# Kernel tuning notes

Measured on AMD Instinct MI355X. Metric: run time of the kernel, lower is better.

## Reference

```python
import jax, jax.numpy as jnp
import numpy as np

N = 2048        # tokens (batch*seq)
H = 4096        # hidden_size (LLaMA-7B)
I = 11008       # intermediate_size (LLaMA-7B)
QMAX = 127.0    # int8 symmetric quant range


def setup_inputs() -> dict:
    key = jax.random.key(0)
    ks = jax.random.split(key, 6)
    # pre-quantized int8 activations (stored as int32) + per-token dynamic scales
    x_q = jax.random.randint(ks[0], (N, H), -127, 128, dtype=jnp.int32)
    x_scale = jax.random.uniform(ks[1], (N,), dtype=jnp.float32) * 0.01 + 1e-4
    # fused [gate; up] int8 weight [2I, H] with per-output-channel scales
    w_gateup = jax.random.randint(ks[2], (2 * I, H), -127, 128, dtype=jnp.int32)
    w_gateup_scale = jax.random.uniform(ks[3], (2 * I,), dtype=jnp.float32) * 0.005 + 1e-4
    # down_proj int8 weight [H, I] with per-output-channel scales
    w_down = jax.random.randint(ks[4], (H, I), -127, 128, dtype=jnp.int32)
    w_down_scale = jax.random.uniform(ks[5], (H,), dtype=jnp.float32) * 0.005 + 1e-4
    return {"x_q": x_q, "x_scale": x_scale, "w_gateup": w_gateup,
            "w_gateup_scale": w_gateup_scale, "w_down": w_down,
            "w_down_scale": w_down_scale}


def reference(x_q, x_scale, w_gateup, w_gateup_scale, w_down, w_down_scale):
    acc = jnp.matmul(x_q, w_gateup.T)                      # [N, 2I] int32
    gateup = acc.astype(jnp.float32) * x_scale[:, None] * w_gateup_scale[None, :]
    # --- fused silu_and_mul + dynamic per-token requantization ---
    gate, up = jnp.split(gateup, 2, axis=-1)               # each [N, I]
    act = jax.nn.silu(gate) * up                           # [N, I]
    s2 = jnp.max(jnp.abs(act), axis=-1) / QMAX             # [N] dynamic scale
    q2 = jnp.clip(jnp.round(act / s2[:, None]), -QMAX, QMAX)  # requantized int8 (as f32)
    out = jnp.matmul(q2, w_down.T.astype(jnp.float32)) * s2[:, None] * w_down_scale[None, :]
    return out                                             # [N, H]
```

## Files before the change

### kernel.cpp

```cpp
#include <hip/hip_runtime.h>
#include <stdint.h>

typedef int i32x4 __attribute__((ext_vector_type(4)));
typedef unsigned short u16x8 __attribute__((ext_vector_type(8)));

#define N_TOK 2048
#define HID   4096
#define INTER 11008
#define TWOI  22016
#define KT1   64
#define KT2   172

#define GLD16(gp, lp) __builtin_amdgcn_global_load_lds( \
    (const __attribute__((address_space(1))) void*)(gp), \
    (__attribute__((address_space(3))) void*)(lp), 16, 0, 0)
#define BAR() __builtin_amdgcn_s_barrier()
#define WVM(n) asm volatile("s_waitcnt vmcnt(" #n ")" ::: "memory")
#define LGKM0() do { asm volatile("s_waitcnt lgkmcnt(0)" ::: "memory"); \
                     __builtin_amdgcn_sched_barrier(0); } while (0)

__device__ __forceinline__ unsigned short f2bf(float f) {
  uint32_t u = __float_as_uint(f);
  uint32_t r = (u + 0x7fffu + ((u >> 16) & 1u)) >> 16;
  return (unsigned short)r;
}

__device__ __forceinline__ float bf2f(unsigned short b) {
  return __uint_as_float(((uint32_t)b) << 16);
}

__global__ __launch_bounds__(256) void pack_panel3(
    const int* __restrict__ src, uint8_t* __restrict__ dst,
    int lgPR, int KT, int K)
{
  const int u = blockIdx.x * 256 + threadIdx.x;
  const int q = u & 3;
  const int r2 = u >> 2;
  const int rl = r2 & ((1 << lgPR) - 1);
  const int s = r2 >> lgPR;
  const int p = s / KT;
  const int t = s - p * KT;
  const int row = (p << lgPR) + rl;
  const int col = t * 64 + ((q ^ (rl & 3)) << 4);
  const int* sp = src + (size_t)row * K + col;
  i32x4 o;
#pragma unroll
  for (int qq = 0; qq < 4; ++qq) {
    i32x4 w = *reinterpret_cast<const i32x4*>(sp + qq * 4);
    o[qq] = (w[0] & 255) | ((w[1] & 255) << 8) | ((w[2] & 255) << 16)
          | ((w[3] & 255) << 24);
  }
  *reinterpret_cast<i32x4*>(dst + (size_t)u * 16) = o;
}

__global__ __launch_bounds__(512, 2) void gemm1_k(
    const uint8_t* __restrict__ x8p, const uint8_t* __restrict__ wgp,
    const float* __restrict__ xs, const float* __restrict__ wgs,
    unsigned short* __restrict__ gu)
{
  __shared__ uint8_t sm[131072];
  const int tid = threadIdx.x;
  const int lane = tid & 63, wid = tid >> 6;
  const int wgm = wid >> 2, wgn = wid & 3;
  const int r15 = lane & 15;
  const int slotC = (((lane >> 4) ^ (r15 & 3)) << 4);

  const int bid = blockIdx.x;
  const int v = (bid & 7) * 86 + (bid >> 3);
  const int mt = v & 7;
  const int ntB = v >> 3;

  const uint8_t* pA = x8p + (size_t)mt  * (KT1 * 16384) + tid * 16;
  const uint8_t* pB = wgp + (size_t)ntB * (KT1 * 16384) + tid * 16;

  const int arow = (wgm << 7) + r15;
  const int brow = (wgn << 6) + r15;
  i32x4 acc[8][4] = {};

#define STG1(t, s) do {                                        \
    uint8_t* l = sm + (s) * 32768 + tid * 16;                  \
    const uint8_t* aa = pA + (size_t)(t) * 16384;              \
    GLD16(aa, l);                                              \
    GLD16(aa + 8192, l + 8192);                                \
    const uint8_t* bb = pB + (size_t)(t) * 16384;              \
    GLD16(bb, l + 16384);                                      \
    GLD16(bb + 8192, l + 24576);                               \
  } while (0)

  STG1(0, 0); STG1(1, 1); STG1(2, 2);
  WVM(8); BAR();

  for (int t = 0; t < KT1; ++t) {
    const int rem = KT1 - 1 - t;
    const uint8_t* b = sm + (t & 3) * 32768;
    uint8_t* lnx = sm + ((t + 3) & 3) * 32768 + tid * 16;
    i32x4 bv[4], av[4];
#pragma unroll
    for (int n = 0; n < 4; ++n)
      bv[n] = *reinterpret_cast<const i32x4*>(
          b + 16384 + (brow + n * 16) * 64 + slotC);
#pragma unroll
    for (int m = 0; m < 4; ++m)
      av[m] = *reinterpret_cast<const i32x4*>(b + (arow + m * 16) * 64 + slotC);
    if (rem >= 3) {
      const uint8_t* bb = pB + (size_t)(t + 3) * 16384;
      GLD16(bb, lnx + 16384);
      GLD16(bb + 8192, lnx + 24576);
    }
    BAR();
    LGKM0();
    __builtin_amdgcn_s_setprio(1);
#pragma unroll
    for (int m = 0; m < 4; ++m)
#pragma unroll
      for (int n = 0; n < 4; ++n)
        acc[m][n] = __builtin_amdgcn_mfma_i32_16x16x64_i8(
            av[m], bv[n], acc[m][n], 0, 0, 0);
    __builtin_amdgcn_s_setprio(0);
#pragma unroll
    for (int m = 0; m < 4; ++m)
      av[m] = *reinterpret_cast<const i32x4*>(
          b + (arow + (m + 4) * 16) * 64 + slotC);
    if (rem >= 3) {
      const uint8_t* aa = pA + (size_t)(t + 3) * 16384;
      GLD16(aa, lnx);
      GLD16(aa + 8192, lnx + 8192);
      WVM(8);
    } else if (rem == 2) { WVM(4); }
    else if (rem == 1)   { WVM(0); }
    BAR();
    LGKM0();
    __builtin_amdgcn_s_setprio(1);
#pragma unroll
    for (int m = 0; m < 4; ++m)
#pragma unroll
      for (int n = 0; n < 4; ++n)
        acc[m + 4][n] = __builtin_amdgcn_mfma_i32_16x16x64_i8(
            av[m], bv[n], acc[m + 4][n], 0, 0, 0);
    __builtin_amdgcn_s_setprio(0);
  }
#undef STG1

  const int rq = (lane >> 4) << 2;
#pragma unroll
  for (int m = 0; m < 8; ++m) {
#pragma unroll
    for (int r = 0; r < 4; ++r) {
      const int rowl = (wgm << 7) + m * 16 + rq + r;
      const int grow = mt * 256 + rowl;
      const float xr = xs[grow];
      const int colb = ntB * 256 + (wgn << 6) + r15;
      unsigned short* op = gu + (size_t)grow * TWOI + colb;
      const float* wp = wgs + colb;
#pragma unroll
      for (int n = 0; n < 4; ++n)
        op[n * 16] = f2bf((float)acc[m][n][r] * xr * wp[n * 16]);
    }
  }
}

__global__ __launch_bounds__(256) void rowmax_k(
    const unsigned short* __restrict__ gu, float* __restrict__ mx)
{
  const int row = blockIdx.x;
  const unsigned short* gp = gu + (size_t)row * TWOI;
  float m = 0.f;
  for (int i = threadIdx.x; i < INTER / 8; i += 256) {
    u16x8 gv = *reinterpret_cast<const u16x8*>(gp + i * 8);
    u16x8 uv = *reinterpret_cast<const u16x8*>(gp + INTER + i * 8);
#pragma unroll
    for (int j = 0; j < 8; ++j) {
      float gf = bf2f(gv[j]);
      float uf = bf2f(uv[j]);
      float a = (gf / (1.f + __expf(-gf))) * uf;
      m = fmaxf(m, __builtin_fabsf(a));
    }
  }
#pragma unroll
  for (int o = 32; o; o >>= 1) m = fmaxf(m, __shfl_xor(m, o, 64));
  __shared__ float red[4];
  const int lane = threadIdx.x & 63, wid = threadIdx.x >> 6;
  if (lane == 0) red[wid] = m;
  __syncthreads();
  if (threadIdx.x == 0)
    mx[row] = fmaxf(fmaxf(red[0], red[1]), fmaxf(red[2], red[3]));
}

__global__ __launch_bounds__(256) void quant_k(
    const unsigned short* __restrict__ gu, const float* __restrict__ mx,
    uint8_t* __restrict__ q2p)
{
  const int u = blockIdx.x * 256 + threadIdx.x;
  const int q = u & 3;
  const int rl = (u >> 2) & 127;
  const int s = u >> 9;
  const int mt = s / KT2;
  const int t = s - mt * KT2;
  const int row = mt * 128 + rl;
  const int col = t * 64 + ((q ^ (rl & 3)) << 4);
  const unsigned short* gp = gu + (size_t)row * TWOI + col;
  const float inv = 127.0f / fmaxf(mx[row], 1e-30f);
  u16x8 g0 = *reinterpret_cast<const u16x8*>(gp);
  u16x8 g1 = *reinterpret_cast<const u16x8*>(gp + 8);
  u16x8 u0 = *reinterpret_cast<const u16x8*>(gp + INTER);
  u16x8 u1 = *reinterpret_cast<const u16x8*>(gp + INTER + 8);
  i32x4 o;
#pragma unroll
  for (int qq = 0; qq < 4; ++qq) {
    uint32_t d = 0;
#pragma unroll
    for (int b = 0; b < 4; ++b) {
      const int j = qq * 4 + b;
      float gf = bf2f((j < 8) ? g0[j] : g1[j - 8]);
      float uf = bf2f((j < 8) ? u0[j] : u1[j - 8]);
      float a = (gf / (1.f + __expf(-gf))) * uf;
      float rr = rintf(a * inv);
      rr = fminf(fmaxf(rr, -127.f), 127.f);
      d |= ((uint32_t)((int)rr & 255)) << (8 * b);
    }
    o[qq] = (int)d;
  }
  *reinterpret_cast<i32x4*>(q2p + (size_t)u * 16) = o;
}

__global__ __launch_bounds__(512, 2) void gemm2_k(
    const uint8_t* __restrict__ q2p, const uint8_t* __restrict__ wdp,
    const float* __restrict__ mx, const float* __restrict__ wds,
    float* __restrict__ out)
{
  __shared__ uint8_t sm[98304];
  const int tid = threadIdx.x;
  const int lane = tid & 63, wid = tid >> 6;
  const int wgm = wid >> 2, wgn = wid & 3;
  const int r15 = lane & 15;
  const int slotC = (((lane >> 4) ^ (r15 & 3)) << 4);

  const int bid = blockIdx.x;
  const int v = (bid & 7) * 32 + (bid >> 3);
  const int nt = v >> 4, mt = v & 15;

  const uint8_t* pA = q2p + (size_t)mt * (KT2 * 8192)  + tid * 16;
  const uint8_t* pB = wdp + (size_t)nt * (KT2 * 16384) + tid * 16;

  const int arow = (wgm << 6) + r15;
  const int brow = (wgn << 6) + r15;
  i32x4 acc[4][4] = {};

#define STG2(t, s) do {                                        \
    uint8_t* l = sm + (s) * 24576 + tid * 16;                  \
    GLD16(pA + (size_t)(t) * 8192, l);                         \
    const uint8_t* bb = pB + (size_t)(t) * 16384;              \
    GLD16(bb, l + 8192);                                       \
    GLD16(bb + 8192, l + 16384);                               \
  } while (0)

  STG2(0, 0); STG2(1, 1); STG2(2, 2);
  WVM(6); BAR();

  for (int t = 0; t < KT2; ++t) {
    const int rem = KT2 - 1 - t;
    const uint8_t* b = sm + (t & 3) * 24576;
    uint8_t* lnx = sm + ((t + 3) & 3) * 24576 + tid * 16;
    i32x4 bv[4], av[2];
#pragma unroll
    for (int n = 0; n < 4; ++n)
      bv[n] = *reinterpret_cast<const i32x4*>(
          b + 8192 + (brow + n * 16) * 64 + slotC);
#pragma unroll
    for (int m = 0; m < 2; ++m)
      av[m] = *reinterpret_cast<const i32x4*>(b + (arow + m * 16) * 64 + slotC);
    if (rem >= 3) {
      const uint8_t* bb = pB + (size_t)(t + 3) * 16384;
      GLD16(bb, lnx + 8192);
      GLD16(bb + 8192, lnx + 16384);
    }
    BAR();
    LGKM0();
    __builtin_amdgcn_s_setprio(1);
#pragma unroll
    for (int m = 0; m < 2; ++m)
#pragma unroll
      for (int n = 0; n < 4; ++n)
        acc[m][n] = __builtin_amdgcn_mfma_i32_16x16x64_i8(
            av[m], bv[n], acc[m][n], 0, 0, 0);
    __builtin_amdgcn_s_setprio(0);
#pragma unroll
    for (int m = 0; m < 2; ++m)
      av[m] = *reinterpret_cast<const i32x4*>(
          b + (arow + (m + 2) * 16) * 64 + slotC);
    if (rem >= 3) {
      GLD16(pA + (size_t)(t + 3) * 8192, lnx);
      WVM(6);
    } else if (rem == 2) { WVM(3); }
    else if (rem == 1)   { WVM(0); }
    BAR();
    LGKM0();
    __builtin_amdgcn_s_setprio(1);
#pragma unroll
    for (int m = 0; m < 2; ++m)
#pragma unroll
      for (int n = 0; n < 4; ++n)
        acc[m + 2][n] = __builtin_amdgcn_mfma_i32_16x16x64_i8(
            av[m], bv[n], acc[m + 2][n], 0, 0, 0);
    __builtin_amdgcn_s_setprio(0);
  }
#undef STG2

  const int rq = (lane >> 4) << 2;
#pragma unroll
  for (int m = 0; m < 4; ++m) {
#pragma unroll
    for (int r = 0; r < 4; ++r) {
      const int rowl = (wgm << 6) + m * 16 + rq + r;
      const int grow = mt * 128 + rowl;
      const float s2 = mx[grow] * (1.0f / 127.0f);
      float* op = out + (size_t)grow * HID + nt * 256 + (wgn << 6) + r15;
      const float* wp = wds + nt * 256 + (wgn << 6) + r15;
#pragma unroll
      for (int n = 0; n < 4; ++n)
        op[n * 16] = (float)acc[m][n][r] * s2 * wp[n * 16];
    }
  }
}

extern "C" void kernel_launch(void* const* d_in, const int* in_sizes, int n_in,
                              void* d_out, int out_size, void* d_ws, size_t ws_size,
                              hipStream_t stream)
{
  const int*   x_q = (const int*)d_in[0];
  const float* xs  = (const float*)d_in[1];
  const int*   wg  = (const int*)d_in[2];
  const float* wgs = (const float*)d_in[3];
  const int*   wd  = (const int*)d_in[4];
  const float* wds = (const float*)d_in[5];
  float* out = (float*)d_out;

  uint8_t* ws = (uint8_t*)d_ws;
  uint8_t* x8p = ws;
  uint8_t* wgp = x8p + 8388608;
  uint8_t* wdp = wgp + 90177536;
  unsigned short* gu = (unsigned short*)(wdp + 45088768);
  float* mx = (float*)((uint8_t*)gu + 90177536);
  uint8_t* q2p = (uint8_t*)mx + 8192;

  pack_panel3<<<2048, 256, 0, stream>>>(x_q, x8p, 8, KT1, HID);
  pack_panel3<<<22016, 256, 0, stream>>>(wg, wgp, 8, KT1, HID);
  pack_panel3<<<11008, 256, 0, stream>>>(wd, wdp, 8, KT2, INTER);

  gemm1_k<<<688, 512, 0, stream>>>(x8p, wgp, xs, wgs, gu);
  rowmax_k<<<N_TOK, 256, 0, stream>>>(gu, mx);
  quant_k<<<5504, 256, 0, stream>>>(gu, mx, q2p);
  gemm2_k<<<256, 512, 0, stream>>>(q2p, wdp, mx, wds, out);
}
```

Measured before the change: 439.8 us.

## Fuse SiLU-mul and row-max into gemm1 epilogue via interleaved gate/up packing

The gate/up weights are repacked so each 256-column tile of gemm1 holds 128 gate and 128 matching up columns. The epilogue then computes silu(gate)*up in-tile through shared memory, writes only the bf16 activation (half the intermediate size), and reduces per-row abs-max with atomicMax. This removes the separate rowmax kernel and halves the intermediate traffic into quant_k. In exchange it adds a shared-memory staging pass, half the waves idling during each epilogue phase, and atomics on mx.

```diff
diff --git a/kernel.cpp b/kernel.cpp
--- a/kernel.cpp
+++ b/kernel.cpp
@@ -53,10 +53,38 @@
   *reinterpret_cast<i32x4*>(dst + (size_t)u * 16) = o;
 }
 
+__global__ __launch_bounds__(256) void pack_gateup(
+    const int* __restrict__ src, uint8_t* __restrict__ dst)
+{
+  const int u = blockIdx.x * 256 + threadIdx.x;
+  const int q = u & 3;
+  const int r2 = u >> 2;
+  const int rl = r2 & 255;
+  const int s = r2 >> 8;
+  const int p = s / KT1;
+  const int t = s - p * KT1;
+  const int srow = (rl < 128) ? (p * 128 + rl) : (INTER + p * 128 + rl - 128);
+  const int col = t * 64 + ((q ^ (rl & 3)) << 4);
+  const int* sp = src + (size_t)srow * HID + col;
+  i32x4 o;
+#pragma unroll
+  for (int qq = 0; qq < 4; ++qq) {
+    i32x4 w = *reinterpret_cast<const i32x4*>(sp + qq * 4);
+    o[qq] = (w[0] & 255) | ((w[1] & 255) << 8) | ((w[2] & 255) << 16)
+          | ((w[3] & 255) << 24);
+  }
+  *reinterpret_cast<i32x4*>(dst + (size_t)u * 16) = o;
+}
+
+__global__ __launch_bounds__(1024) void zero_mx(float* __restrict__ mx) {
+  const int i = blockIdx.x * 1024 + threadIdx.x;
+  if (i < N_TOK) mx[i] = 0.0f;
+}
+
 __global__ __launch_bounds__(512, 2) void gemm1_k(
     const uint8_t* __restrict__ x8p, const uint8_t* __restrict__ wgp,
     const float* __restrict__ xs, const float* __restrict__ wgs,
-    unsigned short* __restrict__ gu)
+    unsigned short* __restrict__ act, float* __restrict__ mx)
 {
   __shared__ uint8_t sm[131072];
   const int tid = threadIdx.x;
@@ -141,53 +169,63 @@
   }
 #undef STG1
 
+  __syncthreads();
+  float* gs = (float*)sm;
   const int rq = (lane >> 4) << 2;
-#pragma unroll
-  for (int m = 0; m < 8; ++m) {
-#pragma unroll
-    for (int r = 0; r < 4; ++r) {
-      const int rowl = (wgm << 7) + m * 16 + rq + r;
-      const int grow = mt * 256 + rowl;
-      const float xr = xs[grow];
-      const int colb = ntB * 256 + (wgn << 6) + r15;
-      unsigned short* op = gu + (size_t)grow * TWOI + colb;
-      const float* wp = wgs + colb;
-#pragma unroll
-      for (int n = 0; n < 4; ++n)
-        op[n * 16] = f2bf((float)acc[m][n][r] * xr * wp[n * 16]);
-    }
-  }
-}
-
-__global__ __launch_bounds__(256) void rowmax_k(
-    const unsigned short* __restrict__ gu, float* __restrict__ mx)
-{
-  const int row = blockIdx.x;
-  const unsigned short* gp = gu + (size_t)row * TWOI;
-  float m = 0.f;
-  for (int i = threadIdx.x; i < INTER / 8; i += 256) {
-    u16x8 gv = *reinterpret_cast<const u16x8*>(gp + i * 8);
-    u16x8 uv = *reinterpret_cast<const u16x8*>(gp + INTER + i * 8);
-#pragma unroll
-    for (int j = 0; j < 8; ++j) {
-      float gf = bf2f(gv[j]);
-      float uf = bf2f(uv[j]);
-      float a = (gf / (1.f + __expf(-gf))) * uf;
-      m = fmaxf(m, __builtin_fabsf(a));
-    }
-  }
-#pragma unroll
-  for (int o = 32; o; o >>= 1) m = fmaxf(m, __shfl_xor(m, o, 64));
-  __shared__ float red[4];
-  const int lane = threadIdx.x & 63, wid = threadIdx.x >> 6;
-  if (lane == 0) red[wid] = m;
+  if (wgn < 2) {
+#pragma unroll
+    for (int m = 0; m < 8; ++m) {
+#pragma unroll
+      for (int n = 0; n < 4; ++n) {
+        const int coll = (wgn << 6) + n * 16 + r15;
+        const float wsc = wgs[ntB * 128 + coll];
+#pragma unroll
+        for (int r = 0; r < 4; ++r) {
+          const int rowl = (wgm << 7) + m * 16 + rq + r;
+          const float g = (float)acc[m][n][r] * xs[mt * 256 + rowl] * wsc;
+          gs[rowl * 128 + (coll ^ (((rowl >> 2) & 1) << 4))] = g;
+        }
+      }
+    }
+  }
   __syncthreads();
-  if (threadIdx.x == 0)
-    mx[row] = fmaxf(fmaxf(red[0], red[1]), fmaxf(red[2], red[3]));
+  if (wgn >= 2) {
+#pragma unroll
+    for (int m = 0; m < 8; ++m) {
+      float am[4] = {0.f, 0.f, 0.f, 0.f};
+#pragma unroll
+      for (int n = 0; n < 4; ++n) {
+        const int cu = ((wgn - 2) << 6) + n * 16 + r15;
+        const float wsc = wgs[INTER + ntB * 128 + cu];
+#pragma unroll
+        for (int r = 0; r < 4; ++r) {
+          const int rowl = (wgm << 7) + m * 16 + rq + r;
+          const int grow = mt * 256 + rowl;
+          const float uv = (float)acc[m][n][r] * xs[grow] * wsc;
+          const float g = gs[rowl * 128 + (cu ^ (((rowl >> 2) & 1) << 4))];
+          const float a = g / (1.f + __expf(-g)) * uv;
+          act[(size_t)grow * INTER + ntB * 128 + cu] = f2bf(a);
+          am[r] = fmaxf(am[r], __builtin_fabsf(a));
+        }
+      }
+#pragma unroll
+      for (int r = 0; r < 4; ++r) {
+#pragma unroll
+        for (int off = 1; off < 16; off <<= 1)
+          am[r] = fmaxf(am[r], __shfl_xor(am[r], off, 64));
+      }
+      if (r15 == 0) {
+#pragma unroll
+        for (int r = 0; r < 4; ++r)
+          atomicMax((int*)&mx[mt * 256 + (wgm << 7) + m * 16 + rq + r],
+                    __float_as_int(am[r]));
+      }
+    }
+  }
 }
 
 __global__ __launch_bounds__(256) void quant_k(
-    const unsigned short* __restrict__ gu, const float* __restrict__ mx,
+    const unsigned short* __restrict__ act, const float* __restrict__ mx,
     uint8_t* __restrict__ q2p)
 {
   const int u = blockIdx.x * 256 + threadIdx.x;
@@ -198,12 +236,10 @@
   const int t = s - mt * KT2;
   const int row = mt * 128 + rl;
   const int col = t * 64 + ((q ^ (rl & 3)) << 4);
-  const unsigned short* gp = gu + (size_t)row * TWOI + col;
+  const unsigned short* ap = act + (size_t)row * INTER + col;
   const float inv = 127.0f / fmaxf(mx[row], 1e-30f);
-  u16x8 g0 = *reinterpret_cast<const u16x8*>(gp);
-  u16x8 g1 = *reinterpret_cast<const u16x8*>(gp + 8);
-  u16x8 u0 = *reinterpret_cast<const u16x8*>(gp + INTER);
-  u16x8 u1 = *reinterpret_cast<const u16x8*>(gp + INTER + 8);
+  u16x8 a0 = *reinterpret_cast<const u16x8*>(ap);
+  u16x8 a1 = *reinterpret_cast<const u16x8*>(ap + 8);
   i32x4 o;
 #pragma unroll
   for (int qq = 0; qq < 4; ++qq) {
@@ -211,10 +247,8 @@
 #pragma unroll
     for (int b = 0; b < 4; ++b) {
       const int j = qq * 4 + b;
-      float gf = bf2f((j < 8) ? g0[j] : g1[j - 8]);
-      float uf = bf2f((j < 8) ? u0[j] : u1[j - 8]);
-      float a = (gf / (1.f + __expf(-gf))) * uf;
-      float rr = rintf(a * inv);
+      float af = bf2f((j < 8) ? a0[j] : a1[j - 8]);
+      float rr = rintf(af * inv);
       rr = fminf(fmaxf(rr, -127.f), 127.f);
       d |= ((uint32_t)((int)rr & 255)) << (8 * b);
     }
@@ -339,16 +373,16 @@
   uint8_t* x8p = ws;
   uint8_t* wgp = x8p + 8388608;
   uint8_t* wdp = wgp + 90177536;
-  unsigned short* gu = (unsigned short*)(wdp + 45088768);
-  float* mx = (float*)((uint8_t*)gu + 90177536);
+  unsigned short* act = (unsigned short*)(wdp + 45088768);
+  float* mx = (float*)((uint8_t*)act + 45088768);
   uint8_t* q2p = (uint8_t*)mx + 8192;
 
+  zero_mx<<<2, 1024, 0, stream>>>(mx);
   pack_panel3<<<2048, 256, 0, stream>>>(x_q, x8p, 8, KT1, HID);
-  pack_panel3<<<22016, 256, 0, stream>>>(wg, wgp, 8, KT1, HID);
+  pack_gateup<<<22016, 256, 0, stream>>>(wg, wgp);
   pack_panel3<<<11008, 256, 0, stream>>>(wd, wdp, 8, KT2, INTER);
 
-  gemm1_k<<<688, 512, 0, stream>>>(x8p, wgp, xs, wgs, gu);
-  rowmax_k<<<N_TOK, 256, 0, stream>>>(gu, mx);
-  quant_k<<<5504, 256, 0, stream>>>(gu, mx, q2p);
+  gemm1_k<<<688, 512, 0, stream>>>(x8p, wgp, xs, wgs, act, mx);
+  quant_k<<<5504, 256, 0, stream>>>(act, mx, q2p);
   gemm2_k<<<256, 512, 0, stream>>>(q2p, wdp, mx, wds, out);
 }
```

New measurement: 450.7 us. 2.5% more time.
